# Kernel tuning notes

Measured on AMD Instinct MI355X. Metric: run time of the kernel, lower is better.

Reference implementation:

```python
import jax, jax.numpy as jnp
import numpy as np

B, S, R, C_IN = 1, 1024, 512, 256   # batch, n_seq (MSA rows), n_res, rep1d_extra_feat
H, CH = 8, 32                       # num_heads, attention_num_c (H*CH == C_IN)


def setup_inputs() -> dict:
    key = jax.random.key(0)
    ks = jax.random.split(key, 7)
    scale = 0.02
    return {
        "x1d": jax.random.normal(ks[0], (B, S, R, C_IN), jnp.float32),
        "mask": jnp.ones((B, S, R), jnp.float32),
        "ln_scale": jnp.ones((C_IN,), jnp.float32),
        "ln_bias": jnp.zeros((C_IN,), jnp.float32),
        "Wq": jax.random.normal(ks[1], (C_IN, H * CH), jnp.float32) * scale,
        "Wk": jax.random.normal(ks[2], (C_IN, CH), jnp.float32) * scale,
        "Wv": jax.random.normal(ks[3], (C_IN, CH), jnp.float32) * scale,
        "Wg": jax.random.normal(ks[4], (C_IN, H * CH), jnp.float32) * scale,
        "bg": jnp.zeros((H * CH,), jnp.float32),
        "Wf": jax.random.normal(ks[5], (H * CH, C_IN), jnpp := jnp.float32) * scale if False else jax.random.normal(ks[5], (H * CH, C_IN), jnp.float32) * scale,
        "bf": jnp.zeros((C_IN,), jnp.float32),
    }


def reference(x1d, mask, ln_scale, ln_bias, Wq, Wk, Wv, Wg, bg, Wf, bf):
    # transpose so attention runs over the MSA-row (column) axis
    x = jnp.swapaxes(x1d, -2, -3)          # [B, R, S, C_IN]
    m = jnp.swapaxes(mask, -1, -2)         # [B, R, S]
    # LayerNorm (eps matches torch default 1e-5)
    mu = jnp.mean(x, axis=-1, keepdims=True)
    var = jnp.mean((x - mu) ** 2, axis=-1, keepdims=True)
    xn = (x - mu) * jax.lax.rsqrt(var + 1e-5) * ln_scale + ln_bias
    # masked mean over rows -> global query
    q_avg = jnp.sum(xn * m[..., None], axis=-2) / (jnp.sum(m, axis=-1)[..., None] + 1e-10)  # [B,R,C_IN]
    att_bias = (1e9 * (m - 1.0))[..., None, :]                         # [B,R,1,S]
    q = (q_avg @ Wq).reshape(*q_avg.shape[:-1], H, CH) * (CH ** -0.5)  # [B,R,H,CH]
    k = xn @ Wk                                                        # [B,R,S,CH]
    v = xn @ Wv                                                        # [B,R,S,CH]
    gate = jax.nn.sigmoid(xn @ Wg + bg).reshape(*xn.shape[:-1], H, CH)  # [B,R,S,H,CH]
    w = jax.nn.softmax(jnp.einsum('brhc,brsc->brhs', q, k) + att_bias, axis=-1)  # [B,R,H,S]
    o = jnp.einsum('brhs,brsc->brhc', w, v)                            # [B,R,H,CH]
    o = o[..., None, :, :] * gate                                      # [B,R,S,H,CH]
    out = o.reshape(*o.shape[:-2], H * CH) @ Wf + bf                   # [B,R,S,C_IN]
    return jnp.swapaxes(out, -2, -3)                                   # [B,S,R,C_IN]
```

## Files before the change

### kernel.cpp

```cpp
#include <hip/hip_runtime.h>
#include <hip/hip_bf16.h>

#define S_DIM 1024
#define R_DIM 512
#define C_DIM 256
#define BS 64
#define SB (S_DIM / BS)

#define XN_OFF (16u << 20)
#define XN_BYTES (512ull * 1024ull * 256ull * 2ull)

typedef __attribute__((ext_vector_type(8))) short short8;
typedef __attribute__((ext_vector_type(8))) unsigned short ushort8v;
typedef __attribute__((ext_vector_type(4))) unsigned short ushort4v;
typedef __attribute__((ext_vector_type(4))) float floatx4;

__device__ inline float bf2f(unsigned short u) {
    return __uint_as_float(((unsigned int)u) << 16);
}
__device__ inline unsigned short f2bf(float f) {
    unsigned int x = __float_as_uint(f);
    unsigned int r = ((x >> 16) & 1u) + 0x7fffu;
    return (unsigned short)((x + r) >> 16);
}

__device__ inline float fast_rcp(float x) {
    float r;
    asm volatile("v_rcp_f32 %0, %1" : "=v"(r) : "v"(x));
    return r;
}

__device__ inline void nt_stf(float* p, float v) {
    __builtin_nontemporal_store(v, p);
}

__device__ inline void async16nt(unsigned short* lds, const unsigned short* g) {
    __builtin_amdgcn_global_load_lds(
        (const __attribute__((address_space(1))) void*)g,
        (__attribute__((address_space(3))) void*)lds, 16, 0, 2);
}

__global__ __launch_bounds__(256) void prep_kernel(
        const float* __restrict__ Wk, const float* __restrict__ Wv,
        const float* __restrict__ Wg, const float* __restrict__ Wf,
        unsigned short* __restrict__ wgT, unsigned short* __restrict__ wfhi,
        unsigned short* __restrict__ wflo, unsigned short* __restrict__ wkvT) {
    int b = blockIdx.x;
    int k = threadIdx.x;
    wgT[b * 256 + k] = f2bf(Wg[k * 256 + b]);
    float w = Wf[k * 256 + b];
    unsigned short hi = f2bf(w);
    wfhi[b * 256 + k] = hi;
    wflo[b * 256 + k] = f2bf(w - bf2f(hi));
    if (b < 64) {
        float t = (b < 32) ? Wk[k * 32 + b] : Wv[k * 32 + (b - 32)];
        wkvT[b * 256 + k] = f2bf(t);
    }
}

__global__ __launch_bounds__(256, 4) void k1a_kernel(
        const float* __restrict__ x, const float* __restrict__ lns,
        const float* __restrict__ lnb, unsigned short* __restrict__ xnws) {
    const int t = threadIdx.x;
    const int row = t >> 3;
    const int q = t & 7;
    const size_t base = ((size_t)blockIdx.x * 32 + row) * 256 + q * 32;
    const floatx4* gp = reinterpret_cast<const floatx4*>(x + base);
    floatx4 v[8];
    float sum = 0.f, sq = 0.f;
#pragma unroll
    for (int i = 0; i < 8; i++) {
        v[i] = gp[i];
        sum += v[i][0] + v[i][1] + v[i][2] + v[i][3];
        sq  += v[i][0] * v[i][0] + v[i][1] * v[i][1]
             + v[i][2] * v[i][2] + v[i][3] * v[i][3];
    }
    sum += __shfl_xor(sum, 1); sq += __shfl_xor(sq, 1);
    sum += __shfl_xor(sum, 2); sq += __shfl_xor(sq, 2);
    sum += __shfl_xor(sum, 4); sq += __shfl_xor(sq, 4);
    float mu = sum * (1.f / 256.f);
    float var = sq * (1.f / 256.f) - mu * mu;
    float rs = rsqrtf(var + 1e-5f);
    const floatx4* sp = reinterpret_cast<const floatx4*>(lns + q * 32);
    const floatx4* bp = reinterpret_cast<const floatx4*>(lnb + q * 32);
    unsigned short* gw = xnws + base;
#pragma unroll
    for (int i = 0; i < 8; i += 2) {
        floatx4 g0 = sp[i],     b0 = bp[i];
        floatx4 g1 = sp[i + 1], b1 = bp[i + 1];
        ushort8v u;
        u[0] = f2bf((v[i][0]     - mu) * rs * g0[0] + b0[0]);
        u[1] = f2bf((v[i][1]     - mu) * rs * g0[1] + b0[1]);
        u[2] = f2bf((v[i][2]     - mu) * rs * g0[2] + b0[2]);
        u[3] = f2bf((v[i][3]     - mu) * rs * g0[3] + b0[3]);
        u[4] = f2bf((v[i + 1][0] - mu) * rs * g1[0] + b1[0]);
        u[5] = f2bf((v[i + 1][1] - mu) * rs * g1[1] + b1[1]);
        u[6] = f2bf((v[i + 1][2] - mu) * rs * g1[2] + b1[2]);
        u[7] = f2bf((v[i + 1][3] - mu) * rs * g1[3] + b1[3]);
        *reinterpret_cast<ushort8v*>(gw + i * 4) = u;
    }
}

__global__ __launch_bounds__(256, 4) void k1b_kernel(
        const unsigned short* __restrict__ xnws, const float* __restrict__ mask,
        const unsigned short* __restrict__ wkvT, unsigned short* __restrict__ kv,
        float* __restrict__ qsum, float* __restrict__ msum) {
    __shared__ unsigned short xn[64 * 256];
    __shared__ float mk[64];
    const int sblk = blockIdx.x, r = blockIdx.y;
    const int s0 = sblk * BS;
    const int t = threadIdx.x;
    const int w = t >> 6, l = t & 63;

    {
        const int c1 = l & 31;
        const int rh = l >> 5;
#pragma unroll
        for (int j = 0; j < 8; j++) {
            int row = w * 16 + 2 * j + rh;
            size_t src = ((size_t)(s0 + row) * R_DIM + r) * C_DIM
                         + (size_t)((c1 ^ (row & 7)) * 8);
            async16nt(xn + (w * 16 + 2 * j) * 256, xnws + src);
        }
    }
    if (t < 64) mk[t] = mask[(size_t)(s0 + t) * R_DIM + r];
    __syncthreads();

    const int lr = l & 15, lk4 = l >> 4;
    const int sw = lr & 7;
    floatx4 acc[4] = {};
#pragma unroll
    for (int kk = 0; kk < 256; kk += 32) {
        const int ch = (((kk >> 3) + lk4) ^ sw) * 8;
        short8 a = *reinterpret_cast<const short8*>(xn + (w * 16 + lr) * 256 + ch);
#pragma unroll
        for (int n = 0; n < 4; n++) {
            short8 b = *reinterpret_cast<const short8*>(wkvT + (n * 16 + lr) * 256 + kk + lk4 * 8);
            acc[n] = __builtin_amdgcn_mfma_f32_16x16x32_bf16(a, b, acc[n], 0, 0, 0);
        }
    }
    unsigned short* kvp = kv + ((size_t)r * S_DIM + s0) * 64;
#pragma unroll
    for (int n = 0; n < 4; n++) {
        int col = n * 16 + lr;
#pragma unroll
        for (int i = 0; i < 4; i++) {
            int row = w * 16 + lk4 * 4 + i;
            kvp[(size_t)row * 64 + col] = f2bf(acc[n][i]);
        }
    }
    {
        const int c = t;
        const int chi = c >> 3, clo = c & 7;
        float cs = 0.f;
#pragma unroll 8
        for (int row = 0; row < 64; row++)
            cs += bf2f(xn[row * 256 + ((chi ^ (row & 7)) * 8 + clo)]) * mk[row];
        qsum[((size_t)r * SB + sblk) * 256 + c] = cs;
    }
    if (t < 64) {
        float m = mk[t];
#pragma unroll
        for (int off = 32; off; off >>= 1) m += __shfl_xor(m, off);
        if (t == 0) msum[r * SB + sblk] = m;
    }
}

__global__ __launch_bounds__(256, 4) void k1_old_kernel(
        const float* __restrict__ x, const float* __restrict__ mask,
        const float* __restrict__ lns, const float* __restrict__ lnb,
        const unsigned short* __restrict__ wkvT, unsigned short* __restrict__ kv,
        float* __restrict__ qsum, float* __restrict__ msum) {
    __shared__ unsigned short xn[64 * 264];
    __shared__ float mk[64];
    const int sblk = blockIdx.x, r = blockIdx.y;
    const int s0 = sblk * BS;
    const int t = threadIdx.x;
    {
        const int row = t >> 2;
        const int q = t & 3;
        const size_t base = ((size_t)(s0 + row) * R_DIM + r) * C_DIM + q * 64;
        const floatx4* gp = reinterpret_cast<const floatx4*>(x + base);
        floatx4 v[16];
        float sum = 0.f, sq = 0.f;
#pragma unroll
        for (int i = 0; i < 16; i++) {
            v[i] = gp[i];
            sum += v[i][0] + v[i][1] + v[i][2] + v[i][3];
            sq  += v[i][0] * v[i][0] + v[i][1] * v[i][1] + v[i][2] * v[i][2] + v[i][3] * v[i][3];
        }
        sum += __shfl_xor(sum, 1); sq += __shfl_xor(sq, 1);
        sum += __shfl_xor(sum, 2); sq += __shfl_xor(sq, 2);
        float mu = sum * (1.f / 256.f);
        float var = sq * (1.f / 256.f) - mu * mu;
        float rs = rsqrtf(var + 1e-5f);
        const floatx4* sp = reinterpret_cast<const floatx4*>(lns + q * 64);
        const floatx4* bp = reinterpret_cast<const floatx4*>(lnb + q * 64);
        unsigned short* wp = xn + row * 264 + q * 64;
#pragma unroll
        for (int i = 0; i < 16; i += 2) {
            floatx4 g0 = sp[i],     b0 = bp[i];
            floatx4 g1 = sp[i + 1], b1 = bp[i + 1];
            ushort8v u;
            u[0] = f2bf((v[i][0]     - mu) * rs * g0[0] + b0[0]);
            u[1] = f2bf((v[i][1]     - mu) * rs * g0[1] + b0[1]);
            u[2] = f2bf((v[i][2]     - mu) * rs * g0[2] + b0[2]);
            u[3] = f2bf((v[i][3]     - mu) * rs * g0[3] + b0[3]);
            u[4] = f2bf((v[i + 1][0] - mu) * rs * g1[0] + b1[0]);
            u[5] = f2bf((v[i + 1][1] - mu) * rs * g1[1] + b1[1]);
            u[6] = f2bf((v[i + 1][2] - mu) * rs * g1[2] + b1[2]);
            u[7] = f2bf((v[i + 1][3] - mu) * rs * g1[3] + b1[3]);
            *reinterpret_cast<ushort8v*>(wp + i * 4) = u;
        }
    }
    if (t < 64) mk[t] = mask[(size_t)(s0 + t) * R_DIM + r];
    __syncthreads();

    const int w = t >> 6, l = t & 63;
    const int lr = l & 15, lk = (l >> 4) * 8;
    floatx4 acc[4] = {};
    const unsigned short* arow = xn + (w * 16 + lr) * 264;
#pragma unroll
    for (int kk = 0; kk < 256; kk += 32) {
        short8 a = *reinterpret_cast<const short8*>(arow + kk + lk);
#pragma unroll
        for (int n = 0; n < 4; n++) {
            short8 b = *reinterpret_cast<const short8*>(wkvT + (n * 16 + lr) * 256 + kk + lk);
            acc[n] = __builtin_amdgcn_mfma_f32_16x16x32_bf16(a, b, acc[n], 0, 0, 0);
        }
    }
    unsigned short* kvp = kv + ((size_t)r * S_DIM + s0) * 64;
#pragma unroll
    for (int n = 0; n < 4; n++) {
        int col = n * 16 + lr;
#pragma unroll
        for (int i = 0; i < 4; i++) {
            int row = w * 16 + (l >> 4) * 4 + i;
            kvp[(size_t)row * 64 + col] = f2bf(acc[n][i]);
        }
    }
    float cs = 0.f;
    const int c = t;
#pragma unroll 8
    for (int row = 0; row < 64; row++) cs += bf2f(xn[row * 264 + c]) * mk[row];
    qsum[((size_t)r * SB + sblk) * 256 + c] = cs;
    if (t < 64) {
        float m = mk[t];
#pragma unroll
        for (int off = 32; off; off >>= 1) m += __shfl_xor(m, off);
        if (t == 0) msum[r * SB + sblk] = m;
    }
}

__global__ __launch_bounds__(256) void k2_kernel(
        const float* __restrict__ mask, const float* __restrict__ Wq,
        const float* __restrict__ qsum, const float* __restrict__ msum,
        const unsigned short* __restrict__ kv, float* __restrict__ oout) {
    __shared__ float qavg[256];
    __shared__ float qh[256];
    __shared__ float lg[8][1024];
    __shared__ float red[8];
    __shared__ unsigned short vt[256 * 36];
    const int r = blockIdx.x;
    const int t = threadIdx.x;

    float ms = 0.f;
#pragma unroll
    for (int i = 0; i < SB; i++) ms += msum[r * SB + i];
    float inv = 1.f / (ms + 1e-10f);
    float qs = 0.f;
#pragma unroll
    for (int i = 0; i < SB; i++) qs += qsum[((size_t)r * SB + i) * 256 + t];
    qavg[t] = qs * inv;
    __syncthreads();

    float accq = 0.f;
#pragma unroll 8
    for (int c = 0; c < 256; c++) accq += qavg[c] * Wq[c * 256 + t];
    qh[t] = accq * 0.17677669529663687f;
    __syncthreads();

    const unsigned short* kvr = kv + (size_t)r * S_DIM * 64;
#pragma unroll
    for (int i = 0; i < 4; i++) {
        int s = i * 256 + t;
        float bias = 1e9f * (mask[(size_t)s * R_DIM + r] - 1.f);
        const unsigned int* kp = reinterpret_cast<const unsigned int*>(kvr + (size_t)s * 64);
        float kvals[32];
#pragma unroll
        for (int j = 0; j < 16; j++) {
            unsigned int u = kp[j];
            kvals[2 * j]     = __uint_as_float(u << 16);
            kvals[2 * j + 1] = __uint_as_float(u & 0xffff0000u);
        }
#pragma unroll
        for (int h = 0; h < 8; h++) {
            float d = 0.f;
#pragma unroll
            for (int ch = 0; ch < 32; ch++) d += qh[h * 32 + ch] * kvals[ch];
            lg[h][s] = d + bias;
        }
    }
    __syncthreads();

    for (int h = 0; h < 8; h++) {
        float mx = -1e30f;
#pragma unroll
        for (int i = 0; i < 4; i++) mx = fmaxf(mx, lg[h][i * 256 + t]);
        for (int off = 32; off; off >>= 1) mx = fmaxf(mx, __shfl_xor(mx, off));
        if ((t & 63) == 0) red[t >> 6] = mx;
        __syncthreads();
        mx = fmaxf(fmaxf(red[0], red[1]), fmaxf(red[2], red[3]));
        float sm = 0.f;
#pragma unroll
        for (int i = 0; i < 4; i++) {
            float e = __expf(lg[h][i * 256 + t] - mx);
            lg[h][i * 256 + t] = e;
            sm += e;
        }
        for (int off = 32; off; off >>= 1) sm += __shfl_xor(sm, off);
        if ((t & 63) == 0) red[4 + (t >> 6)] = sm;
        __syncthreads();
        sm = red[4] + red[5] + red[6] + red[7];
        float isv = 1.f / sm;
#pragma unroll
        for (int i = 0; i < 4; i++) lg[h][i * 256 + t] *= isv;
        __syncthreads();
    }

    const int h = t >> 5, ch = t & 31;
    float o = 0.f;
    for (int st = 0; st < 4; st++) {
        __syncthreads();
        {
            const unsigned short* src = kvr + ((size_t)(st * 256 + t)) * 64 + 32;
            ushort4v* dst = reinterpret_cast<ushort4v*>(vt + t * 36);
#pragma unroll
            for (int j = 0; j < 8; j++)
                dst[j] = *reinterpret_cast<const ushort4v*>(src + 4 * j);
        }
        __syncthreads();
#pragma unroll 8
        for (int sl = 0; sl < 256; sl++)
            o += lg[h][sl + st * 256] * bf2f(vt[sl * 36 + ch]);
    }
    oout[r * 256 + t] = o;
}

__global__ __launch_bounds__(256, 4) void k3r_kernel(
        const float* __restrict__ x, const float* __restrict__ lns,
        const float* __restrict__ lnb, const unsigned short* __restrict__ wgT,
        const unsigned short* __restrict__ wfhi, const unsigned short* __restrict__ wflo,
        const float* __restrict__ oin, const float* __restrict__ bg,
        const float* __restrict__ bfv, float* __restrict__ out) {
    __shared__ unsigned short xa[64 * 264];
    const int sblk = blockIdx.x, r = blockIdx.y;
    const int s0 = sblk * BS;
    const int t = threadIdx.x;
    {
        const int row = t >> 2;
        const int q = t & 3;
        const size_t base = ((size_t)(s0 + row) * R_DIM + r) * C_DIM + q * 64;
        const floatx4* gp = reinterpret_cast<const floatx4*>(x + base);
        floatx4 v[16];
        float sum = 0.f, sq = 0.f;
#pragma unroll
        for (int i = 0; i < 16; i++) {
            v[i] = gp[i];
            sum += v[i][0] + v[i][1] + v[i][2] + v[i][3];
            sq  += v[i][0] * v[i][0] + v[i][1] * v[i][1] + v[i][2] * v[i][2] + v[i][3] * v[i][3];
        }
        sum += __shfl_xor(sum, 1); sq += __shfl_xor(sq, 1);
        sum += __shfl_xor(sum, 2); sq += __shfl_xor(sq, 2);
        float mu = sum * (1.f / 256.f);
        float var = sq * (1.f / 256.f) - mu * mu;
        float rs = rsqrtf(var + 1e-5f);
        const floatx4* sp = reinterpret_cast<const floatx4*>(lns + q * 64);
        const floatx4* bp = reinterpret_cast<const floatx4*>(lnb + q * 64);
        unsigned short* wp = xa + row * 264 + q * 64;
#pragma unroll
        for (int i = 0; i < 16; i += 2) {
            floatx4 g0 = sp[i],     b0 = bp[i];
            floatx4 g1 = sp[i + 1], b1 = bp[i + 1];
            ushort8v u;
            u[0] = f2bf((v[i][0]     - mu) * rs * g0[0] + b0[0]);
            u[1] = f2bf((v[i][1]     - mu) * rs * g0[1] + b0[1]);
            u[2] = f2bf((v[i][2]     - mu) * rs * g0[2] + b0[2]);
            u[3] = f2bf((v[i][3]     - mu) * rs * g0[3] + b0[3]);
            u[4] = f2bf((v[i + 1][0] - mu) * rs * g1[0] + b1[0]);
            u[5] = f2bf((v[i + 1][1] - mu) * rs * g1[1] + b1[1]);
            u[6] = f2bf((v[i + 1][2] - mu) * rs * g1[2] + b1[2]);
            u[7] = f2bf((v[i + 1][3] - mu) * rs * g1[3] + b1[3]);
            *reinterpret_cast<ushort8v*>(wp + i * 4) = u;
        }
    }
    __syncthreads();

    const int w = t >> 6, l = t & 63;
    const int lr = l & 15, lk4 = (l >> 4);
    const int colbase = w * 64;

    float bgv[4], ov[4];
#pragma unroll
    for (int n = 0; n < 4; n++) {
        int col = colbase + n * 16 + lr;
        bgv[n] = bg[col];
        ov[n] = oin[r * 256 + col];
    }

    floatx4 acc[4][4] = {};
#pragma unroll
    for (int kk = 0; kk < 256; kk += 32) {
        short8 a[4];
#pragma unroll
        for (int m = 0; m < 4; m++)
            a[m] = *reinterpret_cast<const short8*>(xa + (m * 16 + lr) * 264 + kk + lk4 * 8);
#pragma unroll
        for (int n = 0; n < 4; n++) {
            short8 b = *reinterpret_cast<const short8*>(wgT + (size_t)(colbase + n * 16 + lr) * 256 + kk + lk4 * 8);
#pragma unroll
            for (int m = 0; m < 4; m++)
                acc[m][n] = __builtin_amdgcn_mfma_f32_16x16x32_bf16(a[m], b, acc[m][n], 0, 0, 0);
        }
    }
    __syncthreads();

#pragma unroll
    for (int m = 0; m < 4; m++) {
#pragma unroll
        for (int n = 0; n < 4; n++) {
            int col = colbase + n * 16 + lr;
#pragma unroll
            for (int i = 0; i < 4; i++) {
                int row = m * 16 + lk4 * 4 + i;
                float e = __expf(-(acc[m][n][i] + bgv[n]));
                float g = fast_rcp(1.f + e);
                xa[row * 264 + col] = f2bf(g * ov[n]);
            }
        }
    }
    __syncthreads();

    floatx4 acc2[4][4] = {};
#pragma unroll
    for (int kk = 0; kk < 256; kk += 32) {
        short8 ah[4];
#pragma unroll
        for (int m = 0; m < 4; m++)
            ah[m] = *reinterpret_cast<const short8*>(xa + (m * 16 + lr) * 264 + kk + lk4 * 8);
#pragma unroll
        for (int n = 0; n < 4; n++) {
            const size_t boff = (size_t)(colbase + n * 16 + lr) * 256 + kk + lk4 * 8;
            short8 bh = *reinterpret_cast<const short8*>(wfhi + boff);
            short8 bl = *reinterpret_cast<const short8*>(wflo + boff);
#pragma unroll
            for (int m = 0; m < 4; m++) {
                acc2[m][n] = __builtin_amdgcn_mfma_f32_16x16x32_bf16(ah[m], bh, acc2[m][n], 0, 0, 0);
                acc2[m][n] = __builtin_amdgcn_mfma_f32_16x16x32_bf16(ah[m], bl, acc2[m][n], 0, 0, 0);
            }
        }
    }

#pragma unroll
    for (int n = 0; n < 4; n++) {
        int col = colbase + n * 16 + lr;
        float bfc = bfv[col];
#pragma unroll
        for (int m = 0; m < 4; m++) {
#pragma unroll
            for (int i = 0; i < 4; i++) {
                int row = m * 16 + lk4 * 4 + i;
                out[((size_t)(s0 + row) * R_DIM + r) * C_DIM + col] = acc2[m][n][i] + bfc;
            }
        }
    }
}

__global__ __launch_bounds__(256, 2) void k3c_kernel(
        const unsigned short* __restrict__ xnws, const unsigned short* __restrict__ wgT,
        const unsigned short* __restrict__ wfhi, const unsigned short* __restrict__ wflo,
        const float* __restrict__ oin, const float* __restrict__ bg,
        const float* __restrict__ bfv, float* __restrict__ out) {
    __shared__ unsigned short xa[2][64 * 256];
    const int sblk = blockIdx.x, r = blockIdx.y;
    const int s0 = sblk * 128;
    const int t = threadIdx.x;
    const int w = t >> 6, l = t & 63;

    {
        const int c1 = l & 31;
        const int rh = l >> 5;
#pragma unroll
        for (int T = 0; T < 2; T++)
#pragma unroll
            for (int j = 0; j < 8; j++) {
                int row = w * 16 + 2 * j + rh;
                size_t src = ((size_t)(s0 + T * 64 + row) * R_DIM + r) * C_DIM
                             + (size_t)((c1 ^ (row & 7)) * 8);
                async16nt(&xa[T][(w * 16 + 2 * j) * 256], xnws + src);
            }
    }

    const int lr = l & 15, lk4 = (l >> 4);
    const int colbase = w * 64;
    const int sw = lr & 7;

    float bgv[4], ov[4], bfc[4];
#pragma unroll
    for (int n = 0; n < 4; n++) {
        int col = colbase + n * 16 + lr;
        bgv[n] = bg[col];
        ov[n] = oin[r * 256 + col];
        bfc[n] = bfv[col];
    }
    __syncthreads();

    floatx4 acc[2][4][4] = {};
    {
        const unsigned short* wgb = wgT + (size_t)(colbase + lr) * 256 + lk4 * 8;
        short8 cw[4], nw[4];
#pragma unroll
        for (int n = 0; n < 4; n++)
            cw[n] = *reinterpret_cast<const short8*>(wgb + n * 4096);
#pragma unroll
        for (int kk = 0; kk < 256; kk += 32) {
            if (kk < 224) {
#pragma unroll
                for (int n = 0; n < 4; n++)
                    nw[n] = *reinterpret_cast<const short8*>(wgb + n * 4096 + kk + 32);
            }
            const int ch = (((kk >> 3) + lk4) ^ sw) * 8;
#pragma unroll
            for (int T = 0; T < 2; T++) {
                short8 a[4];
#pragma unroll
                for (int m = 0; m < 4; m++)
                    a[m] = *reinterpret_cast<const short8*>(&xa[T][(m * 16 + lr) * 256 + ch]);
#pragma unroll
                for (int n = 0; n < 4; n++)
#pragma unroll
                    for (int m = 0; m < 4; m++)
                        acc[T][m][n] = __builtin_amdgcn_mfma_f32_16x16x32_bf16(a[m], cw[n], acc[T][m][n], 0, 0, 0);
            }
            if (kk < 224) {
#pragma unroll
                for (int n = 0; n < 4; n++) cw[n] = nw[n];
            }
        }
    }
    __syncthreads();

#pragma unroll
    for (int T = 0; T < 2; T++)
#pragma unroll
    for (int m = 0; m < 4; m++) {
#pragma unroll
        for (int n = 0; n < 4; n++) {
            int col = colbase + n * 16 + lr;
#pragma unroll
            for (int i = 0; i < 4; i++) {
                int row = m * 16 + lk4 * 4 + i;
                float e = __expf(-(acc[T][m][n][i] + bgv[n]));
                float g = fast_rcp(1.f + e);
                int idx = row * 256 + (((col >> 3) ^ (row & 7)) * 8) + (col & 7);
                xa[T][idx] = f2bf(g * ov[n]);
            }
        }
    }
    __syncthreads();

    floatx4 acc2[2][4][4] = {};
    {
        const unsigned short* whb = wfhi + (size_t)(colbase + lr) * 256 + lk4 * 8;
        const unsigned short* wlb = wflo + (size_t)(colbase + lr) * 256 + lk4 * 8;
        short8 chw[4], clw[4], nhw[4], nlw[4];
#pragma unroll
        for (int n = 0; n < 4; n++) {
            chw[n] = *reinterpret_cast<const short8*>(whb + n * 4096);
            clw[n] = *reinterpret_cast<const short8*>(wlb + n * 4096);
        }
#pragma unroll
        for (int kk = 0; kk < 256; kk += 32) {
            if (kk < 224) {
#pragma unroll
                for (int n = 0; n < 4; n++) {
                    nhw[n] = *reinterpret_cast<const short8*>(whb + n * 4096 + kk + 32);
                    nlw[n] = *reinterpret_cast<const short8*>(wlb + n * 4096 + kk + 32);
                }
            }
            const int ch = (((kk >> 3) + lk4) ^ sw) * 8;
#pragma unroll
            for (int T = 0; T < 2; T++) {
                short8 ah[4];
#pragma unroll
                for (int m = 0; m < 4; m++)
                    ah[m] = *reinterpret_cast<const short8*>(&xa[T][(m * 16 + lr) * 256 + ch]);
#pragma unroll
                for (int n = 0; n < 4; n++)
#pragma unroll
                    for (int m = 0; m < 4; m++) {
                        acc2[T][m][n] = __builtin_amdgcn_mfma_f32_16x16x32_bf16(ah[m], chw[n], acc2[T][m][n], 0, 0, 0);
                        acc2[T][m][n] = __builtin_amdgcn_mfma_f32_16x16x32_bf16(ah[m], clw[n], acc2[T][m][n], 0, 0, 0);
                    }
            }
            if (kk < 224) {
#pragma unroll
                for (int n = 0; n < 4; n++) { chw[n] = nhw[n]; clw[n] = nlw[n]; }
            }
        }
    }

#pragma unroll
    for (int T = 0; T < 2; T++)
#pragma unroll
    for (int n = 0; n < 4; n++) {
        int col = colbase + n * 16 + lr;
#pragma unroll
        for (int m = 0; m < 4; m++) {
#pragma unroll
            for (int i = 0; i < 4; i++) {
                int row = T * 64 + m * 16 + lk4 * 4 + i;
                nt_stf(out + ((size_t)(s0 + row) * R_DIM + r) * C_DIM + col, acc2[T][m][n][i] + bfc[n]);
            }
        }
    }
}

extern "C" void kernel_launch(void* const* d_in, const int* in_sizes, int n_in,
                              void* d_out, int out_size, void* d_ws, size_t ws_size,
                              hipStream_t stream) {
    const float* x1   = (const float*)d_in[0];
    const float* mask = (const float*)d_in[1];
    const float* lns  = (const float*)d_in[2];
    const float* lnb  = (const float*)d_in[3];
    const float* Wq   = (const float*)d_in[4];
    const float* Wk   = (const float*)d_in[5];
    const float* Wv   = (const float*)d_in[6];
    const float* Wg   = (const float*)d_in[7];
    const float* bg   = (const float*)d_in[8];
    const float* Wf   = (const float*)d_in[9];
    const float* bfv  = (const float*)d_in[10];

    char* ws = (char*)d_ws;
    unsigned short* wgT  = (unsigned short*)(ws);
    unsigned short* wfhi = (unsigned short*)(ws + 131072);
    unsigned short* wflo = (unsigned short*)(ws + 262144);
    unsigned short* wkvT = (unsigned short*)(ws + 393216);
    float* qsum = (float*)(ws + 425984);
    float* msum = (float*)(ws + 425984 + 8388608);
    float* oo   = (float*)(ws + 425984 + 8388608 + 32768);
    unsigned short* xnws = (unsigned short*)(ws + XN_OFF);
    unsigned short* kv = (unsigned short*)d_out;
    float* out = (float*)d_out;

    const bool big_ws = ws_size >= (size_t)XN_OFF + (size_t)XN_BYTES;

    prep_kernel<<<256, 256, 0, stream>>>(Wk, Wv, Wg, Wf, wgT, wfhi, wflo, wkvT);
    if (big_ws) {
        k1a_kernel<<<(S_DIM * R_DIM) / 32, 256, 0, stream>>>(x1, lns, lnb, xnws);
        k1b_kernel<<<dim3(SB, R_DIM), 256, 0, stream>>>(xnws, mask, wkvT, kv, qsum, msum);
        k2_kernel<<<R_DIM, 256, 0, stream>>>(mask, Wq, qsum, msum, kv, oo);
        k3c_kernel<<<dim3(SB / 2, R_DIM), 256, 0, stream>>>(xnws, wgT, wfhi, wflo, oo, bg, bfv, out);
    } else {
        k1_old_kernel<<<dim3(SB, R_DIM), 256, 0, stream>>>(x1, mask, lns, lnb, wkvT, kv, qsum, msum);
        k2_kernel<<<R_DIM, 256, 0, stream>>>(mask, Wq, qsum, msum, kv, oo);
        k3r_kernel<<<dim3(SB, R_DIM), 256, 0, stream>>>(x1, lns, lnb, wgT, wfhi, wflo, oo, bg, bfv, out);
    }
}
```

Measured before the change: 801.3 us.

## Transpose MFMA operands for vectorized epilogue stores and per-head softmax

Swaps the A/B operands of the MFMA calls in both GEMMs so each lane holds four consecutive output columns instead of four rows. The gate epilogue can then write packed 4x bf16 values to LDS, and the final output is written with 16-byte non-temporal stores instead of scalar 4-byte stores. The per-row bias, gate-input and output-bias loads become float4 loads. Separately, the k2 softmax gives each 32-thread group one head, which removes the 8-iteration loop with its block-wide barriers and shared reduction array, at the cost of more registers per thread.

```diff
diff --git a/kernel.cpp b/kernel.cpp
--- a/kernel.cpp
+++ b/kernel.cpp
@@ -30,8 +30,8 @@
     return r;
 }
 
-__device__ inline void nt_stf(float* p, float v) {
-    __builtin_nontemporal_store(v, p);
+__device__ inline void nt_st4(float* p, floatx4 v) {
+    __builtin_nontemporal_store(v, reinterpret_cast<floatx4*>(p));
 }
 
 __device__ inline void async16nt(unsigned short* lds, const unsigned short* g) {
@@ -259,7 +259,6 @@
     __shared__ float qavg[256];
     __shared__ float qh[256];
     __shared__ float lg[8][1024];
-    __shared__ float red[8];
     __shared__ unsigned short vt[256 * 36];
     const int r = blockIdx.x;
     const int t = threadIdx.x;
@@ -303,30 +302,32 @@
     }
     __syncthreads();
 
-    for (int h = 0; h < 8; h++) {
+    {
+        const int h = t >> 5;
+        const int g = t & 31;
+        float* lrow = &lg[h][0];
         float mx = -1e30f;
 #pragma unroll
-        for (int i = 0; i < 4; i++) mx = fmaxf(mx, lg[h][i * 256 + t]);
-        for (int off = 32; off; off >>= 1) mx = fmaxf(mx, __shfl_xor(mx, off));
-        if ((t & 63) == 0) red[t >> 6] = mx;
-        __syncthreads();
-        mx = fmaxf(fmaxf(red[0], red[1]), fmaxf(red[2], red[3]));
+        for (int j = 0; j < 32; j++)
+            mx = fmaxf(mx, lrow[g * 32 + ((j + g) & 31)]);
+#pragma unroll
+        for (int off = 16; off; off >>= 1) mx = fmaxf(mx, __shfl_xor(mx, off));
+        float vals[32];
         float sm = 0.f;
 #pragma unroll
-        for (int i = 0; i < 4; i++) {
-            float e = __expf(lg[h][i * 256 + t] - mx);
-            lg[h][i * 256 + t] = e;
+        for (int j = 0; j < 32; j++) {
+            float e = __expf(lrow[g * 32 + ((j + g) & 31)] - mx);
+            vals[j] = e;
             sm += e;
         }
-        for (int off = 32; off; off >>= 1) sm += __shfl_xor(sm, off);
-        if ((t & 63) == 0) red[4 + (t >> 6)] = sm;
-        __syncthreads();
-        sm = red[4] + red[5] + red[6] + red[7];
+#pragma unroll
+        for (int off = 16; off; off >>= 1) sm += __shfl_xor(sm, off);
         float isv = 1.f / sm;
 #pragma unroll
-        for (int i = 0; i < 4; i++) lg[h][i * 256 + t] *= isv;
-        __syncthreads();
-    }
+        for (int j = 0; j < 32; j++)
+            lrow[g * 32 + ((j + g) & 31)] = vals[j] * isv;
+    }
+    __syncthreads();
 
     const int h = t >> 5, ch = t & 31;
     float o = 0.f;
@@ -504,14 +505,14 @@
     const int lr = l & 15, lk4 = (l >> 4);
     const int colbase = w * 64;
     const int sw = lr & 7;
-
-    float bgv[4], ov[4], bfc[4];
+    const int c0 = colbase + lk4 * 4;
+
+    floatx4 bg4[4], ov4[4], bf4[4];
 #pragma unroll
     for (int n = 0; n < 4; n++) {
-        int col = colbase + n * 16 + lr;
-        bgv[n] = bg[col];
-        ov[n] = oin[r * 256 + col];
-        bfc[n] = bfv[col];
+        bg4[n] = *reinterpret_cast<const floatx4*>(bg + c0 + n * 16);
+        ov4[n] = *reinterpret_cast<const floatx4*>(oin + r * 256 + c0 + n * 16);
+        bf4[n] = *reinterpret_cast<const floatx4*>(bfv + c0 + n * 16);
     }
     __syncthreads();
 
@@ -540,7 +541,7 @@
                 for (int n = 0; n < 4; n++)
 #pragma unroll
                     for (int m = 0; m < 4; m++)
-                        acc[T][m][n] = __builtin_amdgcn_mfma_f32_16x16x32_bf16(a[m], cw[n], acc[T][m][n], 0, 0, 0);
+                        acc[T][m][n] = __builtin_amdgcn_mfma_f32_16x16x32_bf16(cw[n], a[m], acc[T][m][n], 0, 0, 0);
             }
             if (kk < 224) {
 #pragma unroll
@@ -554,17 +555,20 @@
     for (int T = 0; T < 2; T++)
 #pragma unroll
     for (int m = 0; m < 4; m++) {
-#pragma unroll
-        for (int n = 0; n < 4; n++) {
-            int col = colbase + n * 16 + lr;
+        const int row = m * 16 + lr;
+        unsigned short* rowp = &xa[T][row * 256];
+#pragma unroll
+        for (int n = 0; n < 4; n++) {
+            const int cb = c0 + n * 16;
+            ushort4v pk;
 #pragma unroll
             for (int i = 0; i < 4; i++) {
-                int row = m * 16 + lk4 * 4 + i;
-                float e = __expf(-(acc[T][m][n][i] + bgv[n]));
+                float e = __expf(-(acc[T][m][n][i] + ((const float*)&bg4[n])[i]));
                 float g = fast_rcp(1.f + e);
-                int idx = row * 256 + (((col >> 3) ^ (row & 7)) * 8) + (col & 7);
-                xa[T][idx] = f2bf(g * ov[n]);
-            }
+                pk[i] = f2bf(g * ((const float*)&ov4[n])[i]);
+            }
+            const int dst = (((cb >> 3) ^ sw) * 8) + (cb & 7);
+            *reinterpret_cast<ushort4v*>(rowp + dst) = pk;
         }
     }
     __syncthreads();
@@ -599,8 +603,8 @@
                 for (int n = 0; n < 4; n++)
 #pragma unroll
                     for (int m = 0; m < 4; m++) {
-                        acc2[T][m][n] = __builtin_amdgcn_mfma_f32_16x16x32_bf16(ah[m], chw[n], acc2[T][m][n], 0, 0, 0);
-                        acc2[T][m][n] = __builtin_amdgcn_mfma_f32_16x16x32_bf16(ah[m], clw[n], acc2[T][m][n], 0, 0, 0);
+                        acc2[T][m][n] = __builtin_amdgcn_mfma_f32_16x16x32_bf16(chw[n], ah[m], acc2[T][m][n], 0, 0, 0);
+                        acc2[T][m][n] = __builtin_amdgcn_mfma_f32_16x16x32_bf16(clw[n], ah[m], acc2[T][m][n], 0, 0, 0);
                     }
             }
             if (kk < 224) {
@@ -613,15 +617,17 @@
 #pragma unroll
     for (int T = 0; T < 2; T++)
 #pragma unroll
-    for (int n = 0; n < 4; n++) {
-        int col = colbase + n * 16 + lr;
-#pragma unroll
-        for (int m = 0; m < 4; m++) {
-#pragma unroll
-            for (int i = 0; i < 4; i++) {
-                int row = T * 64 + m * 16 + lk4 * 4 + i;
-                nt_stf(out + ((size_t)(s0 + row) * R_DIM + r) * C_DIM + col, acc2[T][m][n][i] + bfc[n]);
-            }
+    for (int m = 0; m < 4; m++) {
+        const int row = T * 64 + m * 16 + lr;
+        float* orow = out + ((size_t)(s0 + row) * R_DIM + r) * C_DIM;
+#pragma unroll
+        for (int n = 0; n < 4; n++) {
+            floatx4 o4;
+            o4[0] = acc2[T][m][n][0] + ((const float*)&bf4[n])[0];
+            o4[1] = acc2[T][m][n][1] + ((const float*)&bf4[n])[1];
+            o4[2] = acc2[T][m][n][2] + ((const float*)&bf4[n])[2];
+            o4[3] = acc2[T][m][n][3] + ((const float*)&bf4[n])[3];
+            nt_st4(orow + c0 + n * 16, o4);
         }
     }
 }
```

Result: no change. 808.1 us (+0.9%).
